# Kernel optimization log

Hardware: AMD Instinct MI355X
Metric: run time of the kernel (lower is better)

Reference implementation:

```python
import jax, jax.numpy as jnp
import numpy as np

T, B, I, H, L = 512, 64, 512, 1024, 2


def setup_inputs() -> dict:
    key = jax.random.key(0)
    ks = jax.random.split(key, 11)
    s = 0.03  # keep tanh recurrence in a sane range
    return {
        "x": jax.random.normal(ks[0], (T, B, I), jnp.float32),
        "hidden": jnp.zeros((L, B, H), jnp.float32),
        "W_ih0": jax.random.normal(ks[1], (H, I), jnp.float32) * s,
        "W_hh0": jax.random.normal(ks[2], (H, H), jnp.float32) * s,
        "b_ih0": jax.random.normal(ks[3], (H,), jnp.float32) * s,
        "b_hh0": jax.random.normal(ks[4], (H,), jnp.float32) * s,
        "W_ih1": jax.random.normal(ks[5], (H, H), jnp.float32) * s,
        "W_hh1": jax.random.normal(ks[6], (H, H), jnp.float32) * s,
        "b_ih1": jax.random.normal(ks[7], (H,), jnp.float32) * s,
        "b_hh1": jax.random.normal(ks[8], (H,), jnp.float32) * s,
        "W_fc": jax.random.normal(ks[9], (I, H), jnp.float32) * s,
        "b_fc": jax.random.normal(ks[10], (I,), jnp.float32) * s,
    }


def _rnn_layer(x_proj, h0, W_hh, b_hh):
    # x_proj: [T, B, H] = x @ W_ih.T + b_ih, precomputed as one big GEMM.
    # h_t = tanh(x_proj_t + h_{t-1} @ W_hh.T + b_hh)
    def step(h, xp):
        h_new = jnp.tanh(xp + h @ W_hh.T + b_hh)
        return h_new, h_new
    _, ys = jax.lax.scan(step, h0, x_proj)
    return ys  # [T, B, H]


def reference(x, hidden, W_ih0, W_hh0, b_ih0, b_hh0,
              W_ih1, W_hh1, b_ih1, b_hh1, W_fc, b_fc):
    # Layer 0 (input -> hidden), then layer 1 (hidden -> hidden), tanh RNN.
    out0 = _rnn_layer(jnp.einsum("tbi,hi->tbh", x, W_ih0) + b_ih0,
                      hidden[0], W_hh0, b_hh0)
    out1 = _rnn_layer(jnp.einsum("tbh,gh->tbg", out0, W_ih1) + b_ih1,
                      hidden[1], W_hh1, b_hh1)
    # Trailing Linear(hidden_dim_rnn -> input_size) applied per timestep.
    return jnp.einsum("tbh,ih->tbi", out1, W_fc) + b_fc
```

## Files before the change

kernel.cpp:

```cpp
#include <hip/hip_runtime.h>
#include <stdint.h>

#define T_DIM 512
#define B_DIM 64
#define I_DIM 512
#define H_DIM 1024

typedef __attribute__((ext_vector_type(8))) short short8;
typedef __attribute__((ext_vector_type(4))) float f32x4;

__device__ __forceinline__ unsigned short f2bf(float f) {
    unsigned int u = __float_as_uint(f);
    unsigned int r = (u + 0x7FFFu + ((u >> 16) & 1u)) >> 16;
    return (unsigned short)r;
}
__device__ __forceinline__ float bf2f(unsigned short b) {
    return __uint_as_float(((unsigned int)b) << 16);
}
__device__ __forceinline__ short8 ld_frag(const unsigned short* p) {
    return *reinterpret_cast<const short8*>(p);
}

__global__ void conv_f2bf(const float* __restrict__ in, unsigned short* __restrict__ out, int n4) {
    int i = blockIdx.x * blockDim.x + threadIdx.x;
    int stride = gridDim.x * blockDim.x;
    for (int idx = i; idx < n4; idx += stride) {
        float4 v = reinterpret_cast<const float4*>(in)[idx];
        ushort4 o;
        o.x = f2bf(v.x); o.y = f2bf(v.y); o.z = f2bf(v.z); o.w = f2bf(v.w);
        reinterpret_cast<ushort4*>(out)[idx] = o;
    }
}

__global__ void bias_sum(const float* __restrict__ a, const float* __restrict__ b,
                         float* __restrict__ o, int n) {
    int i = blockIdx.x * blockDim.x + threadIdx.x;
    if (i < n) o[i] = a[i] + b[i];
}

template <int OUT_BF16>
__global__ void gemm_bias(const unsigned short* __restrict__ A,
                          const unsigned short* __restrict__ W,
                          const float* __restrict__ bias,
                          void* __restrict__ Cout,
                          int M, int N, int K) {
    const int ntn = N >> 6;
    const int mt = blockIdx.x / ntn;
    const int nt = blockIdx.x % ntn;
    const int m_base = mt << 6, n_base = nt << 6;
    const int lane = threadIdx.x & 63;
    const int wave = threadIdx.x >> 6;
    const int wm = wave >> 1, wn = wave & 1;
    const int r0 = lane & 15;
    const int g  = lane >> 4;
    const int koff = g << 3;

    f32x4 acc[2][2];
    for (int i = 0; i < 2; i++)
        for (int j = 0; j < 2; j++)
            acc[i][j] = (f32x4)(0.f);

    const unsigned short* Arow0 = A + (size_t)(m_base + wm * 32 + r0) * K + koff;
    const unsigned short* Wrow0 = W + (size_t)(n_base + wn * 32 + r0) * K + koff;

    for (int k0 = 0; k0 < K; k0 += 32) {
        short8 a0 = ld_frag(Arow0 + k0);
        short8 a1 = ld_frag(Arow0 + (size_t)16 * K + k0);
        short8 b0 = ld_frag(Wrow0 + k0);
        short8 b1 = ld_frag(Wrow0 + (size_t)16 * K + k0);
        acc[0][0] = __builtin_amdgcn_mfma_f32_16x16x32_bf16(a0, b0, acc[0][0], 0, 0, 0);
        acc[0][1] = __builtin_amdgcn_mfma_f32_16x16x32_bf16(a0, b1, acc[0][1], 0, 0, 0);
        acc[1][0] = __builtin_amdgcn_mfma_f32_16x16x32_bf16(a1, b0, acc[1][0], 0, 0, 0);
        acc[1][1] = __builtin_amdgcn_mfma_f32_16x16x32_bf16(a1, b1, acc[1][1], 0, 0, 0);
    }

    for (int mi = 0; mi < 2; mi++) {
        for (int ni = 0; ni < 2; ni++) {
            for (int r = 0; r < 4; r++) {
                int row = m_base + wm * 32 + mi * 16 + g * 4 + r;
                int col = n_base + wn * 32 + ni * 16 + r0;
                float v = acc[mi][ni][r] + bias[col];
                if (OUT_BF16)
                    ((unsigned short*)Cout)[(size_t)row * N + col] = f2bf(v);
                else
                    ((float*)Cout)[(size_t)row * N + col] = v;
            }
        }
    }
}

__global__ void rnn_step(int s,
                         const unsigned short* __restrict__ xp0,
                         const unsigned short* __restrict__ whh0,
                         const unsigned short* __restrict__ wih1,
                         const unsigned short* __restrict__ whh1,
                         const float* __restrict__ bias1,
                         const unsigned short* __restrict__ hinit,
                         unsigned short* __restrict__ out0,
                         unsigned short* __restrict__ out1) {
    const int lane = threadIdx.x & 63;
    const int wave = threadIdx.x >> 6;
    const int r0 = lane & 15;
    const int g  = lane >> 4;
    const int koff = g << 3;
    const size_t BH = (size_t)B_DIM * H_DIM;
    const int brow = wave * 16 + r0;

    if (blockIdx.x < 64) {
        const int t = s;
        if (t >= T_DIM) return;
        const int n0 = blockIdx.x << 4;
        const unsigned short* hprev = (t == 0) ? hinit : out0 + (size_t)(t - 1) * BH;
        f32x4 acc = (f32x4)(0.f);
        const unsigned short* Ap = hprev + (size_t)brow * H_DIM + koff;
        const unsigned short* Wp = whh0 + (size_t)(n0 + r0) * H_DIM + koff;
        for (int k0 = 0; k0 < H_DIM; k0 += 32)
            acc = __builtin_amdgcn_mfma_f32_16x16x32_bf16(ld_frag(Ap + k0), ld_frag(Wp + k0), acc, 0, 0, 0);
        const int col = n0 + r0;
        unsigned short* o = out0 + (size_t)t * BH;
        const unsigned short* xp = xp0 + (size_t)t * BH;
        for (int r = 0; r < 4; r++) {
            int b = wave * 16 + g * 4 + r;
            float v = tanhf(acc[r] + bf2f(xp[(size_t)b * H_DIM + col]));
            o[(size_t)b * H_DIM + col] = f2bf(v);
        }
    } else {
        const int t = s - 1;
        if (t < 0) return;
        const int n0 = (blockIdx.x - 64) << 4;
        const unsigned short* a0 = out0 + (size_t)t * BH;
        const unsigned short* h1 = (t == 0) ? (hinit + BH) : out1 + (size_t)(t - 1) * BH;
        f32x4 acc = (f32x4)(0.f);
        const unsigned short* Ap0 = a0 + (size_t)brow * H_DIM + koff;
        const unsigned short* Wp0 = wih1 + (size_t)(n0 + r0) * H_DIM + koff;
        const unsigned short* Ap1 = h1 + (size_t)brow * H_DIM + koff;
        const unsigned short* Wp1 = whh1 + (size_t)(n0 + r0) * H_DIM + koff;
        for (int k0 = 0; k0 < H_DIM; k0 += 32)
            acc = __builtin_amdgcn_mfma_f32_16x16x32_bf16(ld_frag(Ap0 + k0), ld_frag(Wp0 + k0), acc, 0, 0, 0);
        for (int k0 = 0; k0 < H_DIM; k0 += 32)
            acc = __builtin_amdgcn_mfma_f32_16x16x32_bf16(ld_frag(Ap1 + k0), ld_frag(Wp1 + k0), acc, 0, 0, 0);
        const int col = n0 + r0;
        unsigned short* o = out1 + (size_t)t * BH;
        for (int r = 0; r < 4; r++) {
            int b = wave * 16 + g * 4 + r;
            float v = tanhf(acc[r] + bias1[col]);
            o[(size_t)b * H_DIM + col] = f2bf(v);
        }
    }
}

extern "C" void kernel_launch(void* const* d_in, const int* in_sizes, int n_in,
                              void* d_out, int out_size, void* d_ws, size_t ws_size,
                              hipStream_t stream) {
    const float* x      = (const float*)d_in[0];
    const float* hidden = (const float*)d_in[1];
    const float* W_ih0  = (const float*)d_in[2];
    const float* W_hh0  = (const float*)d_in[3];
    const float* b_ih0  = (const float*)d_in[4];
    const float* b_hh0  = (const float*)d_in[5];
    const float* W_ih1  = (const float*)d_in[6];
    const float* W_hh1  = (const float*)d_in[7];
    const float* b_ih1  = (const float*)d_in[8];
    const float* b_hh1  = (const float*)d_in[9];
    const float* W_fc   = (const float*)d_in[10];
    const float* b_fc   = (const float*)d_in[11];

    char* ws = (char*)d_ws;
    size_t off = 0;
    auto alloc = [&](size_t bytes) -> char* {
        char* p = ws + off;
        off += (bytes + 255) & ~(size_t)255;
        return p;
    };
    const size_t TBH = (size_t)T_DIM * B_DIM * H_DIM;
    const size_t TBI = (size_t)T_DIM * B_DIM * I_DIM;

    unsigned short* xb     = (unsigned short*)alloc(TBI * 2);
    unsigned short* wih0b  = (unsigned short*)alloc((size_t)H_DIM * I_DIM * 2);
    unsigned short* whh0b  = (unsigned short*)alloc((size_t)H_DIM * H_DIM * 2);
    unsigned short* wih1b  = (unsigned short*)alloc((size_t)H_DIM * H_DIM * 2);
    unsigned short* whh1b  = (unsigned short*)alloc((size_t)H_DIM * H_DIM * 2);
    unsigned short* wfcb   = (unsigned short*)alloc((size_t)I_DIM * H_DIM * 2);
    unsigned short* hinitb = (unsigned short*)alloc((size_t)2 * B_DIM * H_DIM * 2);
    float* bias0 = (float*)alloc(H_DIM * 4);
    float* bias1 = (float*)alloc(H_DIM * 4);
    unsigned short* xp0    = (unsigned short*)alloc(TBH * 2);
    unsigned short* out0b  = (unsigned short*)alloc(TBH * 2);
    unsigned short* out1b  = (unsigned short*)alloc(TBH * 2);

    auto conv = [&](const float* in, unsigned short* out, int n) {
        int n4 = n / 4;
        int blocks = (n4 + 255) / 256;
        if (blocks > 2048) blocks = 2048;
        conv_f2bf<<<blocks, 256, 0, stream>>>(in, out, n4);
    };
    conv(x, xb, (int)TBI);
    conv(W_ih0, wih0b, H_DIM * I_DIM);
    conv(W_hh0, whh0b, H_DIM * H_DIM);
    conv(W_ih1, wih1b, H_DIM * H_DIM);
    conv(W_hh1, whh1b, H_DIM * H_DIM);
    conv(W_fc, wfcb, I_DIM * H_DIM);
    conv(hidden, hinitb, 2 * B_DIM * H_DIM);
    bias_sum<<<4, 256, 0, stream>>>(b_ih0, b_hh0, bias0, H_DIM);
    bias_sum<<<4, 256, 0, stream>>>(b_ih1, b_hh1, bias1, H_DIM);

    {
        int M = T_DIM * B_DIM, N = H_DIM, K = I_DIM;
        dim3 grid((M / 64) * (N / 64));
        gemm_bias<1><<<grid, 256, 0, stream>>>(xb, wih0b, bias0, xp0, M, N, K);
    }

    for (int s = 0; s <= T_DIM; ++s)
        rnn_step<<<128, 256, 0, stream>>>(s, xp0, whh0b, wih1b, whh1b, bias1,
                                          hinitb, out0b, out1b);

    {
        int M = T_DIM * B_DIM, N = I_DIM, K = H_DIM;
        dim3 grid((M / 64) * (N / 64));
        gemm_bias<0><<<grid, 256, 0, stream>>>(out1b, wfcb, b_fc, d_out, M, N, K);
    }
}
```

Measured before the change: 9.042 ms.

## Replace per-timestep RNN launches with persistent cooperative kernel using flag sync

Replaces 513 per-step kernel launches with one persistent cooperative kernel of 128 blocks. Each block keeps its slice of the recurrent weights resident in LDS, and blocks synchronise across timesteps through per-block global flags with spin-waits. Layer 1 is pipelined one step behind layer 0. It also swaps tanhf for an exp-based fast tanh and splits accumulation across four MFMA chains. This removes launch overhead and the repeated global weight reads, but adds the risk of spin-wait deadlock if not all blocks are co-resident, and relies on the flags0/flags1 allocations being contiguous so the single memset clears both.

```diff
diff --git a/kernel.cpp b/kernel.cpp
--- a/kernel.cpp
+++ b/kernel.cpp
@@ -5,6 +5,7 @@
 #define B_DIM 64
 #define I_DIM 512
 #define H_DIM 1024
+#define BH ((size_t)B_DIM * H_DIM)
 
 typedef __attribute__((ext_vector_type(8))) short short8;
 typedef __attribute__((ext_vector_type(4))) float f32x4;
@@ -17,8 +18,27 @@
 __device__ __forceinline__ float bf2f(unsigned short b) {
     return __uint_as_float(((unsigned int)b) << 16);
 }
-__device__ __forceinline__ short8 ld_frag(const unsigned short* p) {
-    return *reinterpret_cast<const short8*>(p);
+__device__ __forceinline__ float fast_tanh(float x) {
+    x = fminf(fmaxf(x, -15.f), 15.f);
+    float e = __expf(2.f * x);
+    return (e - 1.f) / (e + 1.f);
+}
+
+__device__ __forceinline__ void wait_group(const int* flags) {
+    if (threadIdx.x < 64) {
+        while (__hip_atomic_load(&flags[threadIdx.x], __ATOMIC_RELAXED,
+                                 __HIP_MEMORY_SCOPE_AGENT) == 0)
+            __builtin_amdgcn_s_sleep(2);
+        __threadfence();
+    }
+    __syncthreads();
+}
+__device__ __forceinline__ void signal_flag(int* flag) {
+    __syncthreads();
+    if (threadIdx.x == 0) {
+        __threadfence();
+        __hip_atomic_store(flag, 1, __ATOMIC_RELAXED, __HIP_MEMORY_SCOPE_AGENT);
+    }
 }
 
 __global__ void conv_f2bf(const float* __restrict__ in, unsigned short* __restrict__ out, int n4) {
@@ -64,10 +84,10 @@
     const unsigned short* Wrow0 = W + (size_t)(n_base + wn * 32 + r0) * K + koff;
 
     for (int k0 = 0; k0 < K; k0 += 32) {
-        short8 a0 = ld_frag(Arow0 + k0);
-        short8 a1 = ld_frag(Arow0 + (size_t)16 * K + k0);
-        short8 b0 = ld_frag(Wrow0 + k0);
-        short8 b1 = ld_frag(Wrow0 + (size_t)16 * K + k0);
+        short8 a0 = *reinterpret_cast<const short8*>(Arow0 + k0);
+        short8 a1 = *reinterpret_cast<const short8*>(Arow0 + (size_t)16 * K + k0);
+        short8 b0 = *reinterpret_cast<const short8*>(Wrow0 + k0);
+        short8 b1 = *reinterpret_cast<const short8*>(Wrow0 + (size_t)16 * K + k0);
         acc[0][0] = __builtin_amdgcn_mfma_f32_16x16x32_bf16(a0, b0, acc[0][0], 0, 0, 0);
         acc[0][1] = __builtin_amdgcn_mfma_f32_16x16x32_bf16(a0, b1, acc[0][1], 0, 0, 0);
         acc[1][0] = __builtin_amdgcn_mfma_f32_16x16x32_bf16(a1, b0, acc[1][0], 0, 0, 0);
@@ -89,62 +109,116 @@
     }
 }
 
-__global__ void rnn_step(int s,
-                         const unsigned short* __restrict__ xp0,
-                         const unsigned short* __restrict__ whh0,
-                         const unsigned short* __restrict__ wih1,
-                         const unsigned short* __restrict__ whh1,
-                         const float* __restrict__ bias1,
-                         const unsigned short* __restrict__ hinit,
-                         unsigned short* __restrict__ out0,
-                         unsigned short* __restrict__ out1) {
+__global__ void __launch_bounds__(256, 1)
+rnn_persist(const unsigned short* __restrict__ xp0,
+            const unsigned short* __restrict__ whh0,
+            const unsigned short* __restrict__ wih1,
+            const unsigned short* __restrict__ whh1,
+            const float* __restrict__ bias1,
+            const unsigned short* __restrict__ hinit,
+            unsigned short* __restrict__ out0,
+            unsigned short* __restrict__ out1,
+            int* __restrict__ flags0,
+            int* __restrict__ flags1)
+{
+    extern __shared__ char smem[];
     const int lane = threadIdx.x & 63;
     const int wave = threadIdx.x >> 6;
     const int r0 = lane & 15;
-    const int g  = lane >> 4;
+    const int g = lane >> 4;
     const int koff = g << 3;
-    const size_t BH = (size_t)B_DIM * H_DIM;
-    const int brow = wave * 16 + r0;
-
-    if (blockIdx.x < 64) {
-        const int t = s;
-        if (t >= T_DIM) return;
-        const int n0 = blockIdx.x << 4;
-        const unsigned short* hprev = (t == 0) ? hinit : out0 + (size_t)(t - 1) * BH;
-        f32x4 acc = (f32x4)(0.f);
-        const unsigned short* Ap = hprev + (size_t)brow * H_DIM + koff;
-        const unsigned short* Wp = whh0 + (size_t)(n0 + r0) * H_DIM + koff;
-        for (int k0 = 0; k0 < H_DIM; k0 += 32)
-            acc = __builtin_amdgcn_mfma_f32_16x16x32_bf16(ld_frag(Ap + k0), ld_frag(Wp + k0), acc, 0, 0, 0);
+    const int wg = blockIdx.x;
+    const int brow = (wave << 4) + r0;
+
+    if (wg < 64) {
+        const int n0 = wg << 4;
+        for (int i = threadIdx.x; i < 2048; i += 256) {
+            const int c = i >> 7, kc = i & 127;
+            short8 v = *reinterpret_cast<const short8*>(
+                whh0 + (size_t)(n0 + c) * H_DIM + (kc << 3));
+            *reinterpret_cast<short8*>(smem + ((((kc << 4) + c)) << 4)) = v;
+        }
+        __syncthreads();
         const int col = n0 + r0;
-        unsigned short* o = out0 + (size_t)t * BH;
-        const unsigned short* xp = xp0 + (size_t)t * BH;
-        for (int r = 0; r < 4; r++) {
-            int b = wave * 16 + g * 4 + r;
-            float v = tanhf(acc[r] + bf2f(xp[(size_t)b * H_DIM + col]));
-            o[(size_t)b * H_DIM + col] = f2bf(v);
+        const char* Bp = smem + (g << 8) + (r0 << 4);
+
+        for (int t = 0; t < T_DIM; ++t) {
+            if (t) wait_group(flags0 + (size_t)(t - 1) * 64);
+            const unsigned short* hp = t ? out0 + (size_t)(t - 1) * BH : hinit;
+            const unsigned short* Ap = hp + (size_t)brow * H_DIM + koff;
+            f32x4 acc[4];
+            acc[0] = acc[1] = acc[2] = acc[3] = (f32x4)(0.f);
+            short8 ar[16];
+            #pragma unroll
+            for (int h = 0; h < 2; ++h) {
+                #pragma unroll
+                for (int i = 0; i < 16; ++i)
+                    ar[i] = *reinterpret_cast<const short8*>(Ap + (h << 9) + (i << 5));
+                #pragma unroll
+                for (int i = 0; i < 16; ++i) {
+                    short8 b = *reinterpret_cast<const short8*>(
+                        Bp + (size_t)((h << 4) + i) * 1024);
+                    acc[i & 3] = __builtin_amdgcn_mfma_f32_16x16x32_bf16(ar[i], b, acc[i & 3], 0, 0, 0);
+                }
+            }
+            f32x4 s = acc[0] + acc[1] + acc[2] + acc[3];
+            const unsigned short* xp = xp0 + (size_t)t * BH;
+            unsigned short* o = out0 + (size_t)t * BH;
+            #pragma unroll
+            for (int r = 0; r < 4; ++r) {
+                const int row = (wave << 4) + (g << 2) + r;
+                float v = fast_tanh(s[r] + bf2f(xp[(size_t)row * H_DIM + col]));
+                o[(size_t)row * H_DIM + col] = f2bf(v);
+            }
+            signal_flag(&flags0[(size_t)t * 64 + wg]);
         }
     } else {
-        const int t = s - 1;
-        if (t < 0) return;
-        const int n0 = (blockIdx.x - 64) << 4;
-        const unsigned short* a0 = out0 + (size_t)t * BH;
-        const unsigned short* h1 = (t == 0) ? (hinit + BH) : out1 + (size_t)(t - 1) * BH;
-        f32x4 acc = (f32x4)(0.f);
-        const unsigned short* Ap0 = a0 + (size_t)brow * H_DIM + koff;
-        const unsigned short* Wp0 = wih1 + (size_t)(n0 + r0) * H_DIM + koff;
-        const unsigned short* Ap1 = h1 + (size_t)brow * H_DIM + koff;
-        const unsigned short* Wp1 = whh1 + (size_t)(n0 + r0) * H_DIM + koff;
-        for (int k0 = 0; k0 < H_DIM; k0 += 32)
-            acc = __builtin_amdgcn_mfma_f32_16x16x32_bf16(ld_frag(Ap0 + k0), ld_frag(Wp0 + k0), acc, 0, 0, 0);
-        for (int k0 = 0; k0 < H_DIM; k0 += 32)
-            acc = __builtin_amdgcn_mfma_f32_16x16x32_bf16(ld_frag(Ap1 + k0), ld_frag(Wp1 + k0), acc, 0, 0, 0);
+        const int wg2 = wg - 64;
+        const int n0 = wg2 << 4;
+        for (int i = threadIdx.x; i < 4096; i += 256) {
+            const int c = i >> 8, kc = i & 255;
+            const unsigned short* src = (kc < 128)
+                ? wih1 + (size_t)(n0 + c) * H_DIM + (kc << 3)
+                : whh1 + (size_t)(n0 + c) * H_DIM + ((kc - 128) << 3);
+            short8 v = *reinterpret_cast<const short8*>(src);
+            *reinterpret_cast<short8*>(smem + ((((kc << 4) + c)) << 4)) = v;
+        }
+        __syncthreads();
         const int col = n0 + r0;
-        unsigned short* o = out1 + (size_t)t * BH;
-        for (int r = 0; r < 4; r++) {
-            int b = wave * 16 + g * 4 + r;
-            float v = tanhf(acc[r] + bias1[col]);
-            o[(size_t)b * H_DIM + col] = f2bf(v);
+        const float b1 = bias1[col];
+        const char* Bp = smem + (g << 8) + (r0 << 4);
+
+        for (int t = 0; t < T_DIM; ++t) {
+            wait_group(flags0 + (size_t)t * 64);
+            if (t) wait_group(flags1 + (size_t)(t - 1) * 64);
+            const unsigned short* a0 = out0 + (size_t)t * BH;
+            const unsigned short* h1 = t ? out1 + (size_t)(t - 1) * BH : hinit + BH;
+            f32x4 acc[4];
+            acc[0] = acc[1] = acc[2] = acc[3] = (f32x4)(0.f);
+            short8 ar[16];
+            #pragma unroll
+            for (int h = 0; h < 4; ++h) {
+                const unsigned short* Ap = ((h < 2) ? a0 : h1)
+                    + (size_t)brow * H_DIM + koff + ((size_t)(h & 1) << 9);
+                #pragma unroll
+                for (int i = 0; i < 16; ++i)
+                    ar[i] = *reinterpret_cast<const short8*>(Ap + (i << 5));
+                #pragma unroll
+                for (int i = 0; i < 16; ++i) {
+                    short8 b = *reinterpret_cast<const short8*>(
+                        Bp + (size_t)((h << 4) + i) * 1024);
+                    acc[i & 3] = __builtin_amdgcn_mfma_f32_16x16x32_bf16(ar[i], b, acc[i & 3], 0, 0, 0);
+                }
+            }
+            f32x4 s = acc[0] + acc[1] + acc[2] + acc[3];
+            unsigned short* o = out1 + (size_t)t * BH;
+            #pragma unroll
+            for (int r = 0; r < 4; ++r) {
+                const int row = (wave << 4) + (g << 2) + r;
+                float v = fast_tanh(s[r] + b1);
+                o[(size_t)row * H_DIM + col] = f2bf(v);
+            }
+            signal_flag(&flags1[(size_t)t * 64 + wg2]);
         }
     }
 }
@@ -187,6 +261,8 @@
     unsigned short* xp0    = (unsigned short*)alloc(TBH * 2);
     unsigned short* out0b  = (unsigned short*)alloc(TBH * 2);
     unsigned short* out1b  = (unsigned short*)alloc(TBH * 2);
+    int* flags0 = (int*)alloc((size_t)T_DIM * 64 * 4);
+    int* flags1 = (int*)alloc((size_t)T_DIM * 64 * 4);
 
     auto conv = [&](const float* in, unsigned short* out, int n) {
         int n4 = n / 4;
@@ -204,15 +280,21 @@
     bias_sum<<<4, 256, 0, stream>>>(b_ih0, b_hh0, bias0, H_DIM);
     bias_sum<<<4, 256, 0, stream>>>(b_ih1, b_hh1, bias1, H_DIM);
 
+    (void)hipMemsetAsync(flags0, 0, (size_t)T_DIM * 64 * 4 * 2, stream);
+
     {
         int M = T_DIM * B_DIM, N = H_DIM, K = I_DIM;
         dim3 grid((M / 64) * (N / 64));
         gemm_bias<1><<<grid, 256, 0, stream>>>(xb, wih0b, bias0, xp0, M, N, K);
     }
 
-    for (int s = 0; s <= T_DIM; ++s)
-        rnn_step<<<128, 256, 0, stream>>>(s, xp0, whh0b, wih1b, whh1b, bias1,
-                                          hinitb, out0b, out1b);
+    {
+        void* args[] = {(void*)&xp0, (void*)&whh0b, (void*)&wih1b, (void*)&whh1b,
+                        (void*)&bias1, (void*)&hinitb, (void*)&out0b, (void*)&out1b,
+                        (void*)&flags0, (void*)&flags1};
+        (void)hipLaunchCooperativeKernel(reinterpret_cast<void*>(rnn_persist),
+                                         dim3(128), dim3(256), args, 65536, stream);
+    }
 
     {
         int M = T_DIM * B_DIM, N = I_DIM, K = H_DIM;
```

Result: faster. 7.922 ms (-12.4%).
